# Performance work log

Measured on AMD Instinct MI355X. Metric: run time of the kernel, lower is better.

Reference implementation:

```python
import jax, jax.numpy as jnp
import numpy as np

SOS = 1
EOS = 2
M = 32  # max_y_seq_len


def gru_cell(x, h, W_ih, W_hh, b_ih, b_hh):
    # torch GRUCell math: gates ordered [r, z, n]
    gi = x @ W_ih.T + b_ih          # [B, 3H]
    gh = h @ W_hh.T + b_hh          # [B, 3H]
    i_r, i_z, i_n = jnp.split(gi, 3, axis=-1)
    h_r, h_z, h_n = jnp.split(gh, 3, axis=-1)
    r = jax.nn.sigmoid(i_r + h_r)
    z = jax.nn.sigmoid(i_z + h_z)
    n = jnp.tanh(i_n + r * h_n)
    return (1.0 - z) * n + z * h


def setup_inputs() -> dict:
    key = jax.random.key(0)
    ks = jax.random.split(key, 12)
    B, H, V = 256, 512, 16000
    s = 0.05  # keep GRU pre-activations in a sane range
    return {
        "sem_f": jax.random.normal(ks[0], (B, H), jnp.float32),
        "emb": jax.random.normal(ks[1], (V, H), jnp.float32) * 0.01,
        "W_ih0": jax.random.normal(ks[2], (3 * H, H), jnp.float32) * s,
        "W_hh0": jax.random.normal(ks[3], (3 * H, H), jnp.float32) * s,
        "b_ih0": jax.random.normal(ks[4], (3 * H,), jnp.float32) * s,
        "b_hh0": jax.random.normal(ks[5], (3 * H,), jnp.float32) * s,
        "W_ih1": jax.random.normal(ks[6], (3 * H, H), jnp.float32) * s,
        "W_hh1": jax.random.normal(ks[7], (3 * H, H), jnp.float32) * s,
        "b_ih1": jax.random.normal(ks[8], (3 * H,), jnp.float32) * s,
        "b_hh1": jax.random.normal(ks[9], (3 * H,), jnp.float32) * s,
        "fc_W": jax.random.normal(ks[10], (V, H), jnp.float32) * s,
        "fc_b": jax.random.normal(ks[11], (V,), jnp.float32) * s,
    }


def reference(sem_f, emb, W_ih0, W_hh0, b_ih0, b_hh0,
              W_ih1, W_hh1, b_ih1, b_hh1, fc_W, fc_b):
    B = sem_f.shape[0]
    # hidden = sem_f repeated for each GRU layer
    h0 = sem_f
    h1 = sem_f
    inputs = jnp.full((B,), SOS, dtype=jnp.int32)
    finished = jnp.zeros((B,), dtype=bool)

    def step(carry, _):
        inputs, h0, h1, finished = carry
        unf = ~finished                         # rows still active this step
        x = emb[inputs]                         # [B, H]
        h0n = gru_cell(x, h0, W_ih0, W_hh0, b_ih0, b_hh0)
        h1n = gru_cell(h0n, h1, W_ih1, W_hh1, b_ih1, b_hh1)
        out = h1n @ fc_W.T + fc_b               # [B, V]
        dec = jnp.argmax(out, axis=1).astype(jnp.int32)
        # emulate unf_idxs advanced-indexing writes: finished rows keep -1 / 0
        decoded_t = jnp.where(unf, dec, -1)
        logits_t = jnp.where(unf[:, None], out, 0.0)
        new_finished = finished | (unf & (dec == EOS))
        # pruned (finished) rows freeze hidden and inputs
        h0 = jnp.where(unf[:, None], h0n, h0)
        h1 = jnp.where(unf[:, None], h1n, h1)
        inputs = jnp.where(unf, dec, inputs)
        return (inputs, h0, h1, new_finished), (decoded_t, logits_t)

    _, (decoded, logits) = jax.lax.scan(step, (inputs, h0, h1, finished),
                                        None, length=M)
    decoded = decoded.T                          # [B, M]
    logits = jnp.transpose(logits, (1, 0, 2))    # [B, M, V]
    mask = decoded != -1
    return decoded, logits, mask
```

## Files before the change

kernel.cpp:

```cpp
#include <hip/hip_runtime.h>
#include <math.h>

#define B_   256
#define H_   512
#define V_   16000
#define M_   32
#define SOS_ 1
#define EOS_ 2
#define INV_SCALE (1.0f/2048.0f)

typedef _Float16 half_t;
typedef _Float16 f16x8 __attribute__((ext_vector_type(8)));
typedef float    f32x4 __attribute__((ext_vector_type(4)));

__device__ __forceinline__ void split_f32(float x, half_t& a, half_t& b) {
    a = (half_t)x;
    b = (half_t)((x - (float)a) * 2048.0f);
}

__global__ __launch_bounds__(256)
void init_kernel(const float* __restrict__ sem_f, const float* __restrict__ emb,
                 float* __restrict__ h0, float* __restrict__ h1,
                 half_t* __restrict__ h0a, half_t* __restrict__ h0b,
                 half_t* __restrict__ h1a, half_t* __restrict__ h1b,
                 half_t* __restrict__ xa,  half_t* __restrict__ xb,
                 int* __restrict__ inputs, int* __restrict__ finished)
{
    const int i = blockIdx.x * 256 + threadIdx.x;
    if (i < B_ * H_) {
        const float v = sem_f[i];
        h0[i] = v; h1[i] = v;
        half_t a, b; split_f32(v, a, b);
        h0a[i] = a; h0b[i] = b;
        h1a[i] = a; h1b[i] = b;
        const int j = i & (H_ - 1);
        const float xv = emb[SOS_ * H_ + j];
        half_t c, d; split_f32(xv, c, d);
        xa[i] = c; xb[i] = d;
    }
    if (i < B_) { inputs[i] = SOS_; finished[i] = 0; }
}

__global__ __launch_bounds__(256)
void gru_gemm_mfma(const half_t* __restrict__ Aia, const half_t* __restrict__ Aib,
                   const half_t* __restrict__ Aha, const half_t* __restrict__ Ahb,
                   const float* __restrict__ W_ih, const float* __restrict__ W_hh,
                   const float* __restrict__ b_ih, const float* __restrict__ b_hh,
                   float* __restrict__ PRE)
{
    const int ct = blockIdx.x;
    const int rt = blockIdx.y;
    const bool is_ih = (ct < 12);
    const int wrow0 = (is_ih ? ct : ct - 12) * 128;
    const int row0  = rt * 32;
    const float* W    = is_ih ? W_ih : W_hh;
    const float* bias = is_ih ? b_ih : b_hh;
    const half_t* Aa  = is_ih ? Aia : Aha;
    const half_t* Ab  = is_ih ? Aib : Ahb;

    __shared__ half_t W0s[128][40];
    __shared__ half_t W1s[128][40];

    const int tid  = threadIdx.x;
    const int w    = tid >> 6;
    const int lane = tid & 63;
    const int ll   = lane & 15;
    const int lg   = lane >> 4;

    const int sc = tid >> 1;
    const int sk = (tid & 1) * 16;
    const float* wp = W + (size_t)(wrow0 + sc) * H_ + sk;

    f32x4 accM[2][2] = {};
    f32x4 accC[2][2] = {};

    for (int k0 = 0; k0 < H_; k0 += 32) {
        const float4 q0 = *(const float4*)(wp + k0);
        const float4 q1 = *(const float4*)(wp + k0 + 4);
        const float4 q2 = *(const float4*)(wp + k0 + 8);
        const float4 q3 = *(const float4*)(wp + k0 + 12);
        const float tmp[16] = {q0.x,q0.y,q0.z,q0.w, q1.x,q1.y,q1.z,q1.w,
                               q2.x,q2.y,q2.z,q2.w, q3.x,q3.y,q3.z,q3.w};
        f16x8 p0a, p0b, p1a, p1b;
#pragma unroll
        for (int i = 0; i < 8; ++i) { half_t a,b; split_f32(tmp[i],   a,b); p0a[i]=a; p1a[i]=b; }
#pragma unroll
        for (int i = 0; i < 8; ++i) { half_t a,b; split_f32(tmp[8+i], a,b); p0b[i]=a; p1b[i]=b; }
        __syncthreads();
        *(f16x8*)&W0s[sc][sk]     = p0a;
        *(f16x8*)&W0s[sc][sk + 8] = p0b;
        *(f16x8*)&W1s[sc][sk]     = p1a;
        *(f16x8*)&W1s[sc][sk + 8] = p1b;
        __syncthreads();

        f16x8 a0[2], a1[2];
#pragma unroll
        for (int rf = 0; rf < 2; ++rf) {
            const size_t off = ((size_t)(row0 + 16*rf + ll) << 9) + k0 + (lg << 3);
            a0[rf] = *(const f16x8*)(Aa + off);
            a1[rf] = *(const f16x8*)(Ab + off);
        }
#pragma unroll
        for (int cf = 0; cf < 2; ++cf) {
            const int c = 32*w + 16*cf + ll;
            const f16x8 b0 = *(const f16x8*)&W0s[c][lg << 3];
            const f16x8 b1 = *(const f16x8*)&W1s[c][lg << 3];
#pragma unroll
            for (int rf = 0; rf < 2; ++rf) {
                accM[rf][cf] = __builtin_amdgcn_mfma_f32_16x16x32_f16(a0[rf], b0, accM[rf][cf], 0,0,0);
                accC[rf][cf] = __builtin_amdgcn_mfma_f32_16x16x32_f16(a0[rf], b1, accC[rf][cf], 0,0,0);
                accC[rf][cf] = __builtin_amdgcn_mfma_f32_16x16x32_f16(a1[rf], b0, accC[rf][cf], 0,0,0);
            }
        }
    }

#pragma unroll
    for (int cf = 0; cf < 2; ++cf) {
        const int cl = 32*w + 16*cf + ll;
        const float bv = bias[wrow0 + cl];
        const int c = ct * 128 + cl;
#pragma unroll
        for (int rf = 0; rf < 2; ++rf) {
#pragma unroll
            for (int r = 0; r < 4; ++r) {
                const int row = row0 + 16*rf + lg*4 + r;
                PRE[(size_t)row * 3072 + c] = accM[rf][cf][r] + accC[rf][cf][r] * INV_SCALE + bv;
            }
        }
    }
}

__global__ __launch_bounds__(256)
void gate_kernel(const float* __restrict__ PRE,
                 float* __restrict__ h,
                 half_t* __restrict__ ha, half_t* __restrict__ hb,
                 const int* __restrict__ finished)
{
    const int idx = blockIdx.x * 256 + threadIdx.x;
    const int b = idx >> 9;
    const int j = idx & 511;
    if (finished[b]) return;
    const float* p = PRE + (size_t)b * 3072;
    const float ir = p[j],        iz = p[512 + j],  in_ = p[1024 + j];
    const float hr = p[1536 + j], hz = p[2048 + j], hn  = p[2560 + j];
    const float r = 1.0f / (1.0f + expf(-(ir + hr)));
    const float z = 1.0f / (1.0f + expf(-(iz + hz)));
    const float n = tanhf(in_ + r * hn);
    const float hv = (1.0f - z) * n + z * h[idx];
    h[idx] = hv;
    half_t a, bb; split_f32(hv, a, bb);
    ha[idx] = a; hb[idx] = bb;
}

__global__ __launch_bounds__(256)
void fc_gemm_mfma(const half_t* __restrict__ Aa, const half_t* __restrict__ Ab,
                  const float* __restrict__ fcW, const float* __restrict__ fcb,
                  const int* __restrict__ finished,
                  float* __restrict__ logits, int t)
{
    const int ct = blockIdx.x;
    const int rt = blockIdx.y;
    const int col0 = ct * 128;
    const int row0 = rt * 64;

    __shared__ half_t W0s[128][40];
    __shared__ half_t W1s[128][40];

    const int tid  = threadIdx.x;
    const int wv   = tid >> 6;
    const int wr   = wv >> 1, wc = wv & 1;
    const int lane = tid & 63;
    const int ll   = lane & 15, lg = lane >> 4;

    const int sc = tid >> 1;
    const int sk = (tid & 1) * 16;
    const float* wp = fcW + (size_t)(col0 + sc) * H_ + sk;

    f32x4 accM[2][4] = {};
    f32x4 accC[2][4] = {};

    for (int k0 = 0; k0 < H_; k0 += 32) {
        const float4 q0 = *(const float4*)(wp + k0);
        const float4 q1 = *(const float4*)(wp + k0 + 4);
        const float4 q2 = *(const float4*)(wp + k0 + 8);
        const float4 q3 = *(const float4*)(wp + k0 + 12);
        const float tmp[16] = {q0.x,q0.y,q0.z,q0.w, q1.x,q1.y,q1.z,q1.w,
                               q2.x,q2.y,q2.z,q2.w, q3.x,q3.y,q3.z,q3.w};
        f16x8 p0a, p0b, p1a, p1b;
#pragma unroll
        for (int i = 0; i < 8; ++i) { half_t a,b; split_f32(tmp[i],   a,b); p0a[i]=a; p1a[i]=b; }
#pragma unroll
        for (int i = 0; i < 8; ++i) { half_t a,b; split_f32(tmp[8+i], a,b); p0b[i]=a; p1b[i]=b; }
        __syncthreads();
        *(f16x8*)&W0s[sc][sk]     = p0a;
        *(f16x8*)&W0s[sc][sk + 8] = p0b;
        *(f16x8*)&W1s[sc][sk]     = p1a;
        *(f16x8*)&W1s[sc][sk + 8] = p1b;
        __syncthreads();

        f16x8 a0[2], a1[2];
#pragma unroll
        for (int rf = 0; rf < 2; ++rf) {
            const size_t off = ((size_t)(row0 + 32*wr + 16*rf + ll) << 9) + k0 + (lg << 3);
            a0[rf] = *(const f16x8*)(Aa + off);
            a1[rf] = *(const f16x8*)(Ab + off);
        }
#pragma unroll
        for (int cf = 0; cf < 4; ++cf) {
            const int c = 64*wc + 16*cf + ll;
            const f16x8 b0 = *(const f16x8*)&W0s[c][lg << 3];
            const f16x8 b1 = *(const f16x8*)&W1s[c][lg << 3];
#pragma unroll
            for (int rf = 0; rf < 2; ++rf) {
                accM[rf][cf] = __builtin_amdgcn_mfma_f32_16x16x32_f16(a0[rf], b0, accM[rf][cf], 0,0,0);
                accC[rf][cf] = __builtin_amdgcn_mfma_f32_16x16x32_f16(a0[rf], b1, accC[rf][cf], 0,0,0);
                accC[rf][cf] = __builtin_amdgcn_mfma_f32_16x16x32_f16(a1[rf], b0, accC[rf][cf], 0,0,0);
            }
        }
    }

    int fin[2][4];
#pragma unroll
    for (int rf = 0; rf < 2; ++rf)
#pragma unroll
        for (int r = 0; r < 4; ++r)
            fin[rf][r] = finished[row0 + 32*wr + 16*rf + lg*4 + r];

#pragma unroll
    for (int cf = 0; cf < 4; ++cf) {
        const int col = col0 + 64*wc + 16*cf + ll;
        const float bv = fcb[col];
#pragma unroll
        for (int rf = 0; rf < 2; ++rf) {
#pragma unroll
            for (int r = 0; r < 4; ++r) {
                const int row = row0 + 32*wr + 16*rf + lg*4 + r;
                const float o = fin[rf][r] ? 0.0f
                    : (accM[rf][cf][r] + accC[rf][cf][r] * INV_SCALE + bv);
                logits[((size_t)row * M_ + t) * V_ + col] = o;
            }
        }
    }
}

__global__ __launch_bounds__(256)
void argmax_finalize(const float* __restrict__ logits, const float* __restrict__ emb,
                     int* __restrict__ inputs, int* __restrict__ finished,
                     float* __restrict__ decoded_out, float* __restrict__ mask_out,
                     half_t* __restrict__ xa, half_t* __restrict__ xb, int t)
{
    const int b = blockIdx.x;
    const int tid = threadIdx.x;
    const float* row = logits + ((size_t)b * M_ + t) * V_;

    float bv = -INFINITY; int bi = 0x7fffffff;
    for (int ii = 0; ii < 16; ++ii) {
        const int i4 = tid + 256 * ii;
        if (i4 < V_ / 4) {
            const float4 v = *(const float4*)(row + 4 * i4);
            const float vv[4] = {v.x, v.y, v.z, v.w};
#pragma unroll
            for (int j = 0; j < 4; ++j) {
                const int idx = 4 * i4 + j;
                if (vv[j] > bv || (vv[j] == bv && idx < bi)) { bv = vv[j]; bi = idx; }
            }
        }
    }
    __shared__ float sv[256];
    __shared__ int   si[256];
    sv[tid] = bv; si[tid] = bi;
    __syncthreads();
    for (int s = 128; s > 0; s >>= 1) {
        if (tid < s) {
            const float v2 = sv[tid + s]; const int i2 = si[tid + s];
            if (v2 > sv[tid] || (v2 == sv[tid] && i2 < si[tid])) { sv[tid] = v2; si[tid] = i2; }
        }
        __syncthreads();
    }
    __shared__ int s_tok;
    if (tid == 0) {
        const int fin = finished[b];
        const int dec = si[0];
        decoded_out[b * M_ + t] = fin ? -1.0f : (float)dec;
        mask_out   [b * M_ + t] = fin ? 0.0f : 1.0f;
        int tok;
        if (!fin) { inputs[b] = dec; if (dec == EOS_) finished[b] = 1; tok = dec; }
        else tok = inputs[b];
        s_tok = tok;
    }
    __syncthreads();
    const int tok = s_tok;
    for (int j = tid; j < H_; j += 256) {
        const float v = emb[(size_t)tok * H_ + j];
        half_t a, bb; split_f32(v, a, bb);
        xa[b * H_ + j] = a; xb[b * H_ + j] = bb;
    }
}

extern "C" void kernel_launch(void* const* d_in, const int* in_sizes, int n_in,
                              void* d_out, int out_size, void* d_ws, size_t ws_size,
                              hipStream_t stream)
{
    const float* sem_f = (const float*)d_in[0];
    const float* emb   = (const float*)d_in[1];
    const float* W_ih0 = (const float*)d_in[2];
    const float* W_hh0 = (const float*)d_in[3];
    const float* b_ih0 = (const float*)d_in[4];
    const float* b_hh0 = (const float*)d_in[5];
    const float* W_ih1 = (const float*)d_in[6];
    const float* W_hh1 = (const float*)d_in[7];
    const float* b_ih1 = (const float*)d_in[8];
    const float* b_hh1 = (const float*)d_in[9];
    const float* fc_W  = (const float*)d_in[10];
    const float* fc_b  = (const float*)d_in[11];

    float* out = (float*)d_out;
    float* decoded_out = out;
    float* logits_out  = out + (size_t)B_ * M_;
    float* mask_out    = out + (size_t)B_ * M_ + (size_t)B_ * M_ * V_;

    float*  ws  = (float*)d_ws;
    float*  h0  = ws;
    float*  h1  = ws + 131072;
    float*  PRE = ws + 262144;
    half_t* h0a = (half_t*)(ws + 1048576);
    half_t* h0b = (half_t*)(ws + 1114112);
    half_t* h1a = (half_t*)(ws + 1179648);
    half_t* h1b = (half_t*)(ws + 1245184);
    half_t* xa  = (half_t*)(ws + 1310720);
    half_t* xb  = (half_t*)(ws + 1376256);
    int*    inputs   = (int*)(ws + 1441792);
    int*    finished = (int*)(ws + 1442048);

    init_kernel<<<(B_ * H_ + 255) / 256, 256, 0, stream>>>(
        sem_f, emb, h0, h1, h0a, h0b, h1a, h1b, xa, xb, inputs, finished);

    const dim3 gruGrid(24, 8);
    const dim3 fcGrid(125, 4);

    for (int t = 0; t < M_; ++t) {
        gru_gemm_mfma<<<gruGrid, 256, 0, stream>>>(
            xa, xb, h0a, h0b, W_ih0, W_hh0, b_ih0, b_hh0, PRE);
        gate_kernel<<<(B_ * H_) / 256, 256, 0, stream>>>(PRE, h0, h0a, h0b, finished);
        gru_gemm_mfma<<<gruGrid, 256, 0, stream>>>(
            h0a, h0b, h1a, h1b, W_ih1, W_hh1, b_ih1, b_hh1, PRE);
        gate_kernel<<<(B_ * H_) / 256, 256, 0, stream>>>(PRE, h1, h1a, h1b, finished);
        fc_gemm_mfma<<<fcGrid, 256, 0, stream>>>(
            h1a, h1b, fc_W, fc_b, finished, logits_out, t);
        argmax_finalize<<<B_, 256, 0, stream>>>(
            logits_out, emb, inputs, finished, decoded_out, mask_out, xa, xb, t);
    }
}
```

Measured before the change: 3.079 ms.

## Pre-split weights to fp16 pairs once and fuse argmax into FC GEMM

```diff
diff --git a/kernel.cpp b/kernel.cpp
--- a/kernel.cpp
+++ b/kernel.cpp
@@ -11,11 +11,29 @@
 
 typedef _Float16 half_t;
 typedef _Float16 f16x8 __attribute__((ext_vector_type(8)));
+typedef _Float16 f16x4 __attribute__((ext_vector_type(4)));
 typedef float    f32x4 __attribute__((ext_vector_type(4)));
 
 __device__ __forceinline__ void split_f32(float x, half_t& a, half_t& b) {
     a = (half_t)x;
     b = (half_t)((x - (float)a) * 2048.0f);
+}
+
+__global__ __launch_bounds__(256)
+void split_weights(const float* __restrict__ src, half_t* __restrict__ hi,
+                   half_t* __restrict__ lo, int n4)
+{
+    const int i = blockIdx.x * 256 + threadIdx.x;
+    if (i >= n4) return;
+    const float4 v = ((const float4*)src)[i];
+    f16x4 a, b;
+    half_t t0, t1;
+    split_f32(v.x, t0, t1); a[0] = t0; b[0] = t1;
+    split_f32(v.y, t0, t1); a[1] = t0; b[1] = t1;
+    split_f32(v.z, t0, t1); a[2] = t0; b[2] = t1;
+    split_f32(v.w, t0, t1); a[3] = t0; b[3] = t1;
+    ((f16x4*)hi)[i] = a;
+    ((f16x4*)lo)[i] = b;
 }
 
 __global__ __launch_bounds__(256)
@@ -44,7 +62,8 @@
 __global__ __launch_bounds__(256)
 void gru_gemm_mfma(const half_t* __restrict__ Aia, const half_t* __restrict__ Aib,
                    const half_t* __restrict__ Aha, const half_t* __restrict__ Ahb,
-                   const float* __restrict__ W_ih, const float* __restrict__ W_hh,
+                   const half_t* __restrict__ Wia, const half_t* __restrict__ Wib,
+                   const half_t* __restrict__ Wha, const half_t* __restrict__ Whb,
                    const float* __restrict__ b_ih, const float* __restrict__ b_hh,
                    float* __restrict__ PRE)
 {
@@ -53,10 +72,11 @@
     const bool is_ih = (ct < 12);
     const int wrow0 = (is_ih ? ct : ct - 12) * 128;
     const int row0  = rt * 32;
-    const float* W    = is_ih ? W_ih : W_hh;
-    const float* bias = is_ih ? b_ih : b_hh;
-    const half_t* Aa  = is_ih ? Aia : Aha;
-    const half_t* Ab  = is_ih ? Aib : Ahb;
+    const float*  bias = is_ih ? b_ih : b_hh;
+    const half_t* Aa   = is_ih ? Aia : Aha;
+    const half_t* Ab   = is_ih ? Aib : Ahb;
+    const half_t* W0   = is_ih ? Wia : Wha;
+    const half_t* W1   = is_ih ? Wib : Whb;
 
     __shared__ half_t W0s[128][40];
     __shared__ half_t W1s[128][40];
@@ -69,28 +89,22 @@
 
     const int sc = tid >> 1;
     const int sk = (tid & 1) * 16;
-    const float* wp = W + (size_t)(wrow0 + sc) * H_ + sk;
+    const half_t* wp0 = W0 + (size_t)(wrow0 + sc) * H_ + sk;
+    const half_t* wp1 = W1 + (size_t)(wrow0 + sc) * H_ + sk;
 
     f32x4 accM[2][2] = {};
     f32x4 accC[2][2] = {};
 
     for (int k0 = 0; k0 < H_; k0 += 32) {
-        const float4 q0 = *(const float4*)(wp + k0);
-        const float4 q1 = *(const float4*)(wp + k0 + 4);
-        const float4 q2 = *(const float4*)(wp + k0 + 8);
-        const float4 q3 = *(const float4*)(wp + k0 + 12);
-        const float tmp[16] = {q0.x,q0.y,q0.z,q0.w, q1.x,q1.y,q1.z,q1.w,
-                               q2.x,q2.y,q2.z,q2.w, q3.x,q3.y,q3.z,q3.w};
-        f16x8 p0a, p0b, p1a, p1b;
-#pragma unroll
-        for (int i = 0; i < 8; ++i) { half_t a,b; split_f32(tmp[i],   a,b); p0a[i]=a; p1a[i]=b; }
-#pragma unroll
-        for (int i = 0; i < 8; ++i) { half_t a,b; split_f32(tmp[8+i], a,b); p0b[i]=a; p1b[i]=b; }
+        const f16x8 s0 = *(const f16x8*)(wp0 + k0);
+        const f16x8 s1 = *(const f16x8*)(wp0 + k0 + 8);
+        const f16x8 s2 = *(const f16x8*)(wp1 + k0);
+        const f16x8 s3 = *(const f16x8*)(wp1 + k0 + 8);
         __syncthreads();
-        *(f16x8*)&W0s[sc][sk]     = p0a;
-        *(f16x8*)&W0s[sc][sk + 8] = p0b;
-        *(f16x8*)&W1s[sc][sk]     = p1a;
-        *(f16x8*)&W1s[sc][sk + 8] = p1b;
+        *(f16x8*)&W0s[sc][sk]     = s0;
+        *(f16x8*)&W0s[sc][sk + 8] = s1;
+        *(f16x8*)&W1s[sc][sk]     = s2;
+        *(f16x8*)&W1s[sc][sk + 8] = s3;
         __syncthreads();
 
         f16x8 a0[2], a1[2];
@@ -154,9 +168,11 @@
 
 __global__ __launch_bounds__(256)
 void fc_gemm_mfma(const half_t* __restrict__ Aa, const half_t* __restrict__ Ab,
-                  const float* __restrict__ fcW, const float* __restrict__ fcb,
+                  const half_t* __restrict__ W0, const half_t* __restrict__ W1,
+                  const float* __restrict__ fcb,
                   const int* __restrict__ finished,
-                  float* __restrict__ logits, int t)
+                  float* __restrict__ logits,
+                  float* __restrict__ pmax, int* __restrict__ pidx, int t)
 {
     const int ct = blockIdx.x;
     const int rt = blockIdx.y;
@@ -165,6 +181,8 @@
 
     __shared__ half_t W0s[128][40];
     __shared__ half_t W1s[128][40];
+    __shared__ float  pmS[64][2];
+    __shared__ int    piS[64][2];
 
     const int tid  = threadIdx.x;
     const int wv   = tid >> 6;
@@ -174,28 +192,22 @@
 
     const int sc = tid >> 1;
     const int sk = (tid & 1) * 16;
-    const float* wp = fcW + (size_t)(col0 + sc) * H_ + sk;
+    const half_t* wp0 = W0 + (size_t)(col0 + sc) * H_ + sk;
+    const half_t* wp1 = W1 + (size_t)(col0 + sc) * H_ + sk;
 
     f32x4 accM[2][4] = {};
     f32x4 accC[2][4] = {};
 
     for (int k0 = 0; k0 < H_; k0 += 32) {
-        const float4 q0 = *(const float4*)(wp + k0);
-        const float4 q1 = *(const float4*)(wp + k0 + 4);
-        const float4 q2 = *(const float4*)(wp + k0 + 8);
-        const float4 q3 = *(const float4*)(wp + k0 + 12);
-        const float tmp[16] = {q0.x,q0.y,q0.z,q0.w, q1.x,q1.y,q1.z,q1.w,
-                               q2.x,q2.y,q2.z,q2.w, q3.x,q3.y,q3.z,q3.w};
-        f16x8 p0a, p0b, p1a, p1b;
-#pragma unroll
-        for (int i = 0; i < 8; ++i) { half_t a,b; split_f32(tmp[i],   a,b); p0a[i]=a; p1a[i]=b; }
-#pragma unroll
-        for (int i = 0; i < 8; ++i) { half_t a,b; split_f32(tmp[8+i], a,b); p0b[i]=a; p1b[i]=b; }
+        const f16x8 s0 = *(const f16x8*)(wp0 + k0);
+        const f16x8 s1 = *(const f16x8*)(wp0 + k0 + 8);
+        const f16x8 s2 = *(const f16x8*)(wp1 + k0);
+        const f16x8 s3 = *(const f16x8*)(wp1 + k0 + 8);
         __syncthreads();
-        *(f16x8*)&W0s[sc][sk]     = p0a;
-        *(f16x8*)&W0s[sc][sk + 8] = p0b;
-        *(f16x8*)&W1s[sc][sk]     = p1a;
-        *(f16x8*)&W1s[sc][sk + 8] = p1b;
+        *(f16x8*)&W0s[sc][sk]     = s0;
+        *(f16x8*)&W0s[sc][sk + 8] = s1;
+        *(f16x8*)&W1s[sc][sk]     = s2;
+        *(f16x8*)&W1s[sc][sk + 8] = s3;
         __syncthreads();
 
         f16x8 a0[2], a1[2];
@@ -226,6 +238,13 @@
         for (int r = 0; r < 4; ++r)
             fin[rf][r] = finished[row0 + 32*wr + 16*rf + lg*4 + r];
 
+    float bvv[2][4];
+    int   bii[2][4];
+#pragma unroll
+    for (int rf = 0; rf < 2; ++rf)
+#pragma unroll
+        for (int r = 0; r < 4; ++r) { bvv[rf][r] = -INFINITY; bii[rf][r] = 0x7fffffff; }
+
 #pragma unroll
     for (int cf = 0; cf < 4; ++cf) {
         const int col = col0 + 64*wc + 16*cf + ll;
@@ -235,42 +254,56 @@
 #pragma unroll
             for (int r = 0; r < 4; ++r) {
                 const int row = row0 + 32*wr + 16*rf + lg*4 + r;
-                const float o = fin[rf][r] ? 0.0f
-                    : (accM[rf][cf][r] + accC[rf][cf][r] * INV_SCALE + bv);
-                logits[((size_t)row * M_ + t) * V_ + col] = o;
-            }
-        }
-    }
-}
-
-__global__ __launch_bounds__(256)
-void argmax_finalize(const float* __restrict__ logits, const float* __restrict__ emb,
+                const float raw = accM[rf][cf][r] + accC[rf][cf][r] * INV_SCALE + bv;
+                logits[((size_t)row * M_ + t) * V_ + col] = fin[rf][r] ? 0.0f : raw;
+                if (raw > bvv[rf][r]) { bvv[rf][r] = raw; bii[rf][r] = col; }
+            }
+        }
+    }
+
+#pragma unroll
+    for (int rf = 0; rf < 2; ++rf) {
+#pragma unroll
+        for (int r = 0; r < 4; ++r) {
+            float v = bvv[rf][r]; int ix = bii[rf][r];
+#pragma unroll
+            for (int m = 1; m < 16; m <<= 1) {
+                const float ov = __shfl_xor(v, m);
+                const int   oi = __shfl_xor(ix, m);
+                if (ov > v || (ov == v && oi < ix)) { v = ov; ix = oi; }
+            }
+            if (ll == 0) {
+                const int lr = 32*wr + 16*rf + lg*4 + r;
+                pmS[lr][wc] = v; piS[lr][wc] = ix;
+            }
+        }
+    }
+    __syncthreads();
+    if (tid < 64) {
+        float v = pmS[tid][0]; int ix = piS[tid][0];
+        const float v2 = pmS[tid][1]; const int i2 = piS[tid][1];
+        if (v2 > v || (v2 == v && i2 < ix)) { v = v2; ix = i2; }
+        pmax[(row0 + tid) * 128 + ct] = v;
+        pidx[(row0 + tid) * 128 + ct] = ix;
+    }
+}
+
+__global__ __launch_bounds__(128)
+void finalize_kernel(const float* __restrict__ pmax, const int* __restrict__ pidx,
+                     const float* __restrict__ emb,
                      int* __restrict__ inputs, int* __restrict__ finished,
                      float* __restrict__ decoded_out, float* __restrict__ mask_out,
                      half_t* __restrict__ xa, half_t* __restrict__ xb, int t)
 {
     const int b = blockIdx.x;
     const int tid = threadIdx.x;
-    const float* row = logits + ((size_t)b * M_ + t) * V_;
-
-    float bv = -INFINITY; int bi = 0x7fffffff;
-    for (int ii = 0; ii < 16; ++ii) {
-        const int i4 = tid + 256 * ii;
-        if (i4 < V_ / 4) {
-            const float4 v = *(const float4*)(row + 4 * i4);
-            const float vv[4] = {v.x, v.y, v.z, v.w};
-#pragma unroll
-            for (int j = 0; j < 4; ++j) {
-                const int idx = 4 * i4 + j;
-                if (vv[j] > bv || (vv[j] == bv && idx < bi)) { bv = vv[j]; bi = idx; }
-            }
-        }
-    }
-    __shared__ float sv[256];
-    __shared__ int   si[256];
-    sv[tid] = bv; si[tid] = bi;
+    __shared__ float sv[128];
+    __shared__ int   si[128];
+    float v = -INFINITY; int ix = 0x7fffffff;
+    if (tid < 125) { v = pmax[b * 128 + tid]; ix = pidx[b * 128 + tid]; }
+    sv[tid] = v; si[tid] = ix;
     __syncthreads();
-    for (int s = 128; s > 0; s >>= 1) {
+    for (int s = 64; s > 0; s >>= 1) {
         if (tid < s) {
             const float v2 = sv[tid + s]; const int i2 = si[tid + s];
             if (v2 > sv[tid] || (v2 == sv[tid] && i2 < si[tid])) { sv[tid] = v2; si[tid] = i2; }
@@ -290,9 +323,9 @@
     }
     __syncthreads();
     const int tok = s_tok;
-    for (int j = tid; j < H_; j += 256) {
-        const float v = emb[(size_t)tok * H_ + j];
-        half_t a, bb; split_f32(v, a, bb);
+    for (int j = tid; j < H_; j += 128) {
+        const float v2 = emb[(size_t)tok * H_ + j];
+        half_t a, bb; split_f32(v2, a, bb);
         xa[b * H_ + j] = a; xb[b * H_ + j] = bb;
     }
 }
@@ -320,17 +353,37 @@
     float* mask_out    = out + (size_t)B_ * M_ + (size_t)B_ * M_ * V_;
 
     float*  ws  = (float*)d_ws;
-    float*  h0  = ws;
-    float*  h1  = ws + 131072;
-    float*  PRE = ws + 262144;
+    float*  PRE = ws;
+    float*  h0  = ws + 786432;
+    float*  h1  = ws + 917504;
     half_t* h0a = (half_t*)(ws + 1048576);
     half_t* h0b = (half_t*)(ws + 1114112);
     half_t* h1a = (half_t*)(ws + 1179648);
     half_t* h1b = (half_t*)(ws + 1245184);
     half_t* xa  = (half_t*)(ws + 1310720);
     half_t* xb  = (half_t*)(ws + 1376256);
-    int*    inputs   = (int*)(ws + 1441792);
-    int*    finished = (int*)(ws + 1442048);
+    float*  pmax = ws + 1441792;
+    int*    pidx = (int*)(ws + 1474560);
+    int*    inputs   = (int*)(ws + 1507328);
+    int*    finished = (int*)(ws + 1507584);
+    half_t* wi0a = (half_t*)(ws + 1507840);
+    half_t* wi0b = (half_t*)(ws + 1901056);
+    half_t* wh0a = (half_t*)(ws + 2294272);
+    half_t* wh0b = (half_t*)(ws + 2687488);
+    half_t* wi1a = (half_t*)(ws + 3080704);
+    half_t* wi1b = (half_t*)(ws + 3473920);
+    half_t* wh1a = (half_t*)(ws + 3867136);
+    half_t* wh1b = (half_t*)(ws + 4260352);
+    half_t* fca  = (half_t*)(ws + 4653568);
+    half_t* fcbp = (half_t*)(ws + 8749568);
+
+    const int nGru4 = (1536 * 512) / 4;
+    const int nFc4  = (V_ * H_) / 4;
+    split_weights<<<(nGru4 + 255) / 256, 256, 0, stream>>>(W_ih0, wi0a, wi0b, nGru4);
+    split_weights<<<(nGru4 + 255) / 256, 256, 0, stream>>>(W_hh0, wh0a, wh0b, nGru4);
+    split_weights<<<(nGru4 + 255) / 256, 256, 0, stream>>>(W_ih1, wi1a, wi1b, nGru4);
+    split_weights<<<(nGru4 + 255) / 256, 256, 0, stream>>>(W_hh1, wh1a, wh1b, nGru4);
+    split_weights<<<(nFc4 + 255) / 256, 256, 0, stream>>>(fc_W, fca, fcbp, nFc4);
 
     init_kernel<<<(B_ * H_ + 255) / 256, 256, 0, stream>>>(
         sem_f, emb, h0, h1, h0a, h0b, h1a, h1b, xa, xb, inputs, finished);
@@ -340,14 +393,14 @@
 
     for (int t = 0; t < M_; ++t) {
         gru_gemm_mfma<<<gruGrid, 256, 0, stream>>>(
-            xa, xb, h0a, h0b, W_ih0, W_hh0, b_ih0, b_hh0, PRE);
+            xa, xb, h0a, h0b, wi0a, wi0b, wh0a, wh0b, b_ih0, b_hh0, PRE);
         gate_kernel<<<(B_ * H_) / 256, 256, 0, stream>>>(PRE, h0, h0a, h0b, finished);
         gru_gemm_mfma<<<gruGrid, 256, 0, stream>>>(
-            h0a, h0b, h1a, h1b, W_ih1, W_hh1, b_ih1, b_hh1, PRE);
+            h0a, h0b, h1a, h1b, wi1a, wi1b, wh1a, wh1b, b_ih1, b_hh1, PRE);
         gate_kernel<<<(B_ * H_) / 256, 256, 0, stream>>>(PRE, h1, h1a, h1b, finished);
         fc_gemm_mfma<<<fcGrid, 256, 0, stream>>>(
-            h1a, h1b, fc_W, fc_b, finished, logits_out, t);
-        argmax_finalize<<<B_, 256, 0, stream>>>(
-            logits_out, emb, inputs, finished, decoded_out, mask_out, xa, xb, t);
-    }
-}
+            h1a, h1b, fca, fcbp, fc_b, finished, logits_out, pmax, pidx, t);
+        finalize_kernel<<<B_, 128, 0, stream>>>(
+            pmax, pidx, emb, inputs, finished, decoded_out, mask_out, xa, xb, t);
+    }
+}
```

After: 2.979 ms. 1.03x faster.
